# Kernel optimization log

Measured on AMD Instinct MI355X. Metric: run time of the kernel, lower is better.

The kernel has to match this reference:

```python
import jax, jax.numpy as jnp
import numpy as np


def _greedy_nms_single(scores, suppress):
    """Greedy score-ordered suppression for one scene.
    scores: [P] float max class score; suppress: [P, P] bool, row i suppresses col j
    (same class AND within class radius of point i). Returns keep mask [P] bool."""
    P = scores.shape[0]

    def cond(state):
        alive, _ = state
        return jnp.any(alive)

    def body(state):
        alive, keep = state
        i = jnp.argmax(jnp.where(alive, scores, -jnp.inf))  # highest-score remaining
        keep = keep.at[i].set(True)
        alive = alive & ~suppress[i]   # drop same-class points within radius of i
        alive = alive.at[i].set(False)
        return alive, keep

    alive0 = jnp.ones((P,), dtype=bool)
    keep0 = jnp.zeros((P,), dtype=bool)
    _, keep = jax.lax.while_loop(cond, body, (alive0, keep0))
    return keep


def _keep_mask(centers, cls_preds, class_radius):
    # centers: [B,P,3], cls_preds: [B,P,K], class_radius: [K]
    scores = jnp.max(cls_preds, axis=-1)     # [B,P]  torch.max(..., dim=1) values
    labels = jnp.argmax(cls_preds, axis=-1)  # [B,P]  torch.max(..., dim=1) indices
    diff = centers[:, :, None, :] - centers[:, None, :, :]        # [B,P,P,3]
    dist = jnp.sqrt(jnp.sum(diff * diff, axis=-1))                # [B,P,P] torch.norm
    same_class = labels[:, :, None] == labels[:, None, :]         # [B,P,P]
    radii = class_radius[labels]                                  # [B,P] radius of keeper i
    suppress = same_class & (dist < radii[:, :, None])            # [B,P,P]
    return jax.vmap(_greedy_nms_single)(scores, suppress)         # [B,P] bool


def setup_inputs() -> dict:
    key = jax.random.key(0)
    k1, k2, k3, k4 = jax.random.split(key, 4)
    B, P, C, K = 8, 2048, 1024, 3
    centers = jax.random.normal(k1, (B, P, 3), dtype=jnp.float32)
    features = jax.random.normal(k2, (B, P, C), dtype=jnp.float32)
    cls_preds = jax.random.normal(k3, (B, P, K), dtype=jnp.float32)
    class_radius = jax.random.uniform(k4, (K,), dtype=jnp.float32)  # per-class NMS radius
    return {"centers": centers, "features": features, "cls_preds": cls_preds,
            "class_radius": class_radius}


def reference(centers, features, cls_preds, class_radius):
    """Greedy per-class radius-based keypoint suppression (fixed-shape variant):
    instead of dynamically gathering kept points (data-dependent shape), we return
    the boolean keep mask and the inputs with suppressed entries zeroed out."""
    keep = _keep_mask(centers, cls_preds, class_radius)      # [B,P] bool
    m = keep[..., None].astype(features.dtype)
    return (centers * m, features * m, cls_preds * m, keep)
```

## Files before the change

### kernel.cpp

```cpp
#include <hip/hip_runtime.h>

#define B 8
#define P 2048
#define C 1024
#define NCHUNK 32
#define FEAT4 (B*P*C/4)
#define CEN4  (B*P*3/4)

typedef unsigned long long u64;
typedef unsigned int u32;

__global__ __launch_bounds__(512) void rank_kernel(
    const float* __restrict__ centers,
    const float* __restrict__ cls_preds,
    float4* __restrict__ scent,
    int* __restrict__ sidx)
{
    __shared__ u64 s_keys[P];
    __shared__ u32 s_cnt[64][9];
    const int b = blockIdx.x >> 5, gi = blockIdx.x & 31;
    const int tid = threadIdx.x, wv = tid >> 6, lane = tid & 63;
    const float* clsb = cls_preds + (size_t)b * P * 3;
    const float* cenb = centers + (size_t)b * P * 3;

    for (int e = tid; e < P; e += 512) {
        float s0 = clsb[e*3], s1 = clsb[e*3+1], s2 = clsb[e*3+2];
        float sc = s0; int lb = 0;
        if (s1 > sc) { sc = s1; lb = 1; }
        if (s2 > sc) { sc = s2; lb = 2; }
        u32 ub = __float_as_uint(sc);
        u32 ord = (ub & 0x80000000u) ? ~ub : (ub | 0x80000000u);
        s_keys[e] = ((u64)(~ord) << 32) | (u32)((e << 2) | lb);
    }
    __syncthreads();

    const u64 myk = s_keys[(gi << 6) + lane];
    u32 c = 0;
    const int sbase = wv << 8;
    #pragma unroll 8
    for (int u = 0; u < 256; ++u)
        c += (s_keys[sbase + u] < myk) ? 1u : 0u;
    s_cnt[lane][wv] = c;
    __syncthreads();

    if (wv == 0) {
        u32 rank = 0;
        #pragma unroll
        for (int s = 0; s < 8; ++s) rank += s_cnt[lane][s];
        u32 lo = (u32)myk;
        int orig = (int)(lo >> 2);
        float4 cc;
        cc.x = cenb[orig*3]; cc.y = cenb[orig*3+1]; cc.z = cenb[orig*3+2];
        cc.w = __int_as_float((int)(lo & 3));
        scent[(size_t)b * P + rank] = cc;
        sidx[(size_t)b * P + rank] = (int)lo;
    }
}

__global__ __launch_bounds__(512) void matrix_kernel(
    const float4* __restrict__ scent,
    const float* __restrict__ class_radius,
    u32* __restrict__ matT)
{
    __shared__ float4 s_cent[P];
    const int b = blockIdx.x >> 5, gi = blockIdx.x & 31;
    const int tid = threadIdx.x, wv = tid >> 6, lane = tid & 63;

    const float4 cj = scent[(size_t)b * P + (gi << 6) + lane];
    const int labj = __float_as_int(cj.w);
    const float r = class_radius[labj];
    const float r2 = r * r;
    const int wmin = gi << 1;

    for (int i = tid; i < P; i += 512) s_cent[i] = scent[(size_t)b * P + i];
    __syncthreads();

    for (int w = wv; w < 64; w += 8) {
        if (w < wmin) continue;
        u32 acc = 0;
        #pragma unroll
        for (int u = 0; u < 32; ++u) {
            float4 ci = s_cent[(w << 5) + u];
            float dx = cj.x - ci.x, dy = cj.y - ci.y, dz = cj.z - ci.z;
            bool sup = (__float_as_int(ci.w) == labj)
                       && (dx*dx + dy*dy + dz*dz < r2);
            acc |= ((u32)sup) << u;
        }
        matT[((size_t)b * 64 + w) * P + (gi << 6) + lane] = acc;
    }
}

__global__ __launch_bounds__(576) void scan_kernel(
    const u32* __restrict__ matT,
    const int* __restrict__ sidx,
    float* __restrict__ out_keep)
{
    __shared__ u32 s_tile[4][64][65];
    __shared__ u32 s_removed[64];
    __shared__ int s_sidx[P];
    const int b = blockIdx.x;
    const int tid = threadIdx.x, wv = tid >> 6, lane = tid & 63;
    const u32* mb = matT + (size_t)b * 64 * P;

    for (int i = tid; i < P; i += 576) s_sidx[i] = sidx[(size_t)b * P + i];
    if (tid < 64) s_removed[tid] = 0;
    if (wv >= 1) {
        #pragma unroll
        for (int c = 0; c < 3; ++c) {
            #pragma unroll
            for (int rr = 0; rr < 8; ++rr) {
                int w = ((wv - 1) << 3) + rr;
                s_tile[c][lane][w] = mb[(size_t)w * P + (c << 6) + lane];
            }
        }
    }
    __syncthreads();

    for (int g = 0; g < NCHUNK; ++g) {
        const int buf = g & 3;
        if (wv >= 1 && g + 3 < NCHUNK) {
            const int nb = (g + 3) << 6;
            #pragma unroll
            for (int rr = 0; rr < 8; ++rr) {
                int w = ((wv - 1) << 3) + rr;
                s_tile[(g + 3) & 3][lane][w] = mb[(size_t)w * P + nb + lane];
            }
        }
        if (wv == 0) {
            const int base = g << 6;
            u64 row = (u64)s_tile[buf][lane][2*g]
                    | ((u64)s_tile[buf][lane][2*g + 1] << 32);
            u64 rem = (u64)s_removed[2*g] | ((u64)s_removed[2*g + 1] << 32);
            u64 alive = ~rem;
            const u64 below = (1ull << lane) - 1ull;
            u64 keepm = 0;
            while (alive) {
                bool ok = ((alive >> lane) & 1ull) && ((row & alive & below) == 0ull);
                u64 newk = __ballot(ok);
                keepm |= newk;
                bool dead = (row & newk) != 0ull;
                u64 deadm = __ballot(dead);
                alive &= ~(newk | deadm);
            }
            int orig = s_sidx[base + lane] >> 2;
            out_keep[(size_t)b * P + orig] = ((keepm >> lane) & 1ull) ? 1.0f : 0.0f;
            u32 acc = 0;
            u64 m = keepm;
            while (m) {
                int q = (int)__ffsll((long long)m) - 1;
                acc |= s_tile[buf][q][lane];
                m &= m - 1ull;
            }
            s_removed[lane] |= acc;
        }
        __syncthreads();
    }
}

__global__ __launch_bounds__(256) void mask_kernel(
    const float* __restrict__ centers,
    const float* __restrict__ features,
    const float* __restrict__ cls_preds,
    const float* __restrict__ keep,
    float* __restrict__ out_centers,
    float* __restrict__ out_feat,
    float* __restrict__ out_cls)
{
    const int idx = blockIdx.x * 256 + threadIdx.x;
    if (idx < FEAT4) {
        const int row = idx >> 8;
        const float m = keep[row];
        float4 v = ((const float4*)features)[idx];
        v.x *= m; v.y *= m; v.z *= m; v.w *= m;
        ((float4*)out_feat)[idx] = v;
    } else if (idx < FEAT4 + CEN4) {
        const int q = idx - FEAT4;
        float4 v = ((const float4*)centers)[q];
        const int e = q * 4;
        v.x *= keep[(e    ) / 3]; v.y *= keep[(e + 1) / 3];
        v.z *= keep[(e + 2) / 3]; v.w *= keep[(e + 3) / 3];
        ((float4*)out_centers)[q] = v;
    } else if (idx < FEAT4 + 2 * CEN4) {
        const int q = idx - FEAT4 - CEN4;
        float4 v = ((const float4*)cls_preds)[q];
        const int e = q * 4;
        v.x *= keep[(e    ) / 3]; v.y *= keep[(e + 1) / 3];
        v.z *= keep[(e + 2) / 3]; v.w *= keep[(e + 3) / 3];
        ((float4*)out_cls)[q] = v;
    }
}

extern "C" void kernel_launch(void* const* d_in, const int* in_sizes, int n_in,
                              void* d_out, int out_size, void* d_ws, size_t ws_size,
                              hipStream_t stream) {
    const float* centers      = (const float*)d_in[0];
    const float* features     = (const float*)d_in[1];
    const float* cls_preds    = (const float*)d_in[2];
    const float* class_radius = (const float*)d_in[3];

    float* out = (float*)d_out;
    float* out_centers = out;
    float* out_feat    = out + (size_t)B * P * 3;
    float* out_cls     = out_feat + (size_t)B * P * C;
    float* out_keep    = out_cls + (size_t)B * P * 3;

    u32*    matT  = (u32*)out_feat;
    float4* scent = (float4*)(out_feat + 1048576);
    int*    sidx  = (int*)(out_feat + 1048576 + 65536);

    hipLaunchKernelGGL(rank_kernel, dim3(B * 32), dim3(512), 0, stream,
                       centers, cls_preds, scent, sidx);
    hipLaunchKernelGGL(matrix_kernel, dim3(B * 32), dim3(512), 0, stream,
                       scent, class_radius, matT);
    hipLaunchKernelGGL(scan_kernel, dim3(B), dim3(576), 0, stream,
                       matT, sidx, out_keep);
    hipLaunchKernelGGL(mask_kernel, dim3((FEAT4 + 2 * CEN4 + 255) / 256), dim3(256),
                       0, stream,
                       centers, features, cls_preds, out_keep,
                       out_centers, out_feat, out_cls);
}
```

Before: 181.1 us.

## Parallelize suppression-row OR across waves with register-held matrix tiles

The scan kernel drops the shared-memory transpose tile. Each helper wave now prefetches its slice of the suppression matrix into registers with vector loads, while wave 0 loads only its diagonal words. After wave 0 resolves a chunk's keep mask, the other eight waves OR the rows of the kept points in parallel into the removed mask using shared atomics. This replaces wave 0's serial ffs loop over shared-memory rows. The keep output is written in one pass at the end. In exchange it adds a second block barrier per chunk and uses strided, poorly coalesced global loads for the prefetch.

Result: faster. 173.0 us (-4.4%).

```diff
diff --git a/kernel.cpp b/kernel.cpp
--- a/kernel.cpp
+++ b/kernel.cpp
@@ -95,41 +95,49 @@
     const int* __restrict__ sidx,
     float* __restrict__ out_keep)
 {
-    __shared__ u32 s_tile[4][64][65];
+    __shared__ int s_sidx[P];
     __shared__ u32 s_removed[64];
-    __shared__ int s_sidx[P];
+    __shared__ u64 s_keepm[NCHUNK];
     const int b = blockIdx.x;
     const int tid = threadIdx.x, wv = tid >> 6, lane = tid & 63;
     const u32* mb = matT + (size_t)b * 64 * P;
 
     for (int i = tid; i < P; i += 576) s_sidx[i] = sidx[(size_t)b * P + i];
     if (tid < 64) s_removed[tid] = 0;
-    if (wv >= 1) {
-        #pragma unroll
-        for (int c = 0; c < 3; ++c) {
-            #pragma unroll
-            for (int rr = 0; rr < 8; ++rr) {
-                int w = ((wv - 1) << 3) + rr;
-                s_tile[c][lane][w] = mb[(size_t)w * P + (c << 6) + lane];
+
+    uint4 Va[4], Vb[4];
+    u32 Ra[4], Rb[4];
+    const int qb = (wv - 1) << 3;
+
+    #pragma unroll
+    for (int c = 0; c < 3; ++c) {
+        if (wv >= 1) {
+            const u32* p = mb + (size_t)lane * P + (c << 6) + qb;
+            Va[c] = *(const uint4*)p;
+            Vb[c] = *(const uint4*)(p + 4);
+        } else {
+            Ra[c] = mb[(size_t)(2*c    ) * P + (c << 6) + lane];
+            Rb[c] = mb[(size_t)(2*c + 1) * P + (c << 6) + lane];
+        }
+    }
+    __syncthreads();
+
+    #pragma unroll
+    for (int g = 0; g < NCHUNK; ++g) {
+        const int slot = g & 3;
+        if (g + 3 < NCHUNK) {
+            const int c = g + 3, ns = c & 3;
+            if (wv >= 1) {
+                const u32* p = mb + (size_t)lane * P + (c << 6) + qb;
+                Va[ns] = *(const uint4*)p;
+                Vb[ns] = *(const uint4*)(p + 4);
+            } else {
+                Ra[ns] = mb[(size_t)(2*c    ) * P + (c << 6) + lane];
+                Rb[ns] = mb[(size_t)(2*c + 1) * P + (c << 6) + lane];
             }
         }
-    }
-    __syncthreads();
-
-    for (int g = 0; g < NCHUNK; ++g) {
-        const int buf = g & 3;
-        if (wv >= 1 && g + 3 < NCHUNK) {
-            const int nb = (g + 3) << 6;
-            #pragma unroll
-            for (int rr = 0; rr < 8; ++rr) {
-                int w = ((wv - 1) << 3) + rr;
-                s_tile[(g + 3) & 3][lane][w] = mb[(size_t)w * P + nb + lane];
-            }
-        }
         if (wv == 0) {
-            const int base = g << 6;
-            u64 row = (u64)s_tile[buf][lane][2*g]
-                    | ((u64)s_tile[buf][lane][2*g + 1] << 32);
+            u64 row = (u64)Ra[slot] | ((u64)Rb[slot] << 32);
             u64 rem = (u64)s_removed[2*g] | ((u64)s_removed[2*g + 1] << 32);
             u64 alive = ~rem;
             const u64 below = (1ull << lane) - 1ull;
@@ -142,18 +150,29 @@
                 u64 deadm = __ballot(dead);
                 alive &= ~(newk | deadm);
             }
-            int orig = s_sidx[base + lane] >> 2;
-            out_keep[(size_t)b * P + orig] = ((keepm >> lane) & 1ull) ? 1.0f : 0.0f;
+            if (lane == 0) s_keepm[g] = keepm;
+        }
+        __syncthreads();
+        if (wv >= 1) {
+            const u32 kb = (u32)(s_keepm[g] >> qb) & 0xffu;
             u32 acc = 0;
-            u64 m = keepm;
-            while (m) {
-                int q = (int)__ffsll((long long)m) - 1;
-                acc |= s_tile[buf][q][lane];
-                m &= m - 1ull;
-            }
-            s_removed[lane] |= acc;
+            if (kb & 0x01u) acc |= Va[slot].x;
+            if (kb & 0x02u) acc |= Va[slot].y;
+            if (kb & 0x04u) acc |= Va[slot].z;
+            if (kb & 0x08u) acc |= Va[slot].w;
+            if (kb & 0x10u) acc |= Vb[slot].x;
+            if (kb & 0x20u) acc |= Vb[slot].y;
+            if (kb & 0x40u) acc |= Vb[slot].z;
+            if (kb & 0x80u) acc |= Vb[slot].w;
+            if (acc) atomicOr(&s_removed[lane], acc);
         }
         __syncthreads();
+    }
+
+    for (int pos = tid; pos < P; pos += 576) {
+        u64 km = s_keepm[pos >> 6];
+        int orig = s_sidx[pos] >> 2;
+        out_keep[(size_t)b * P + orig] = ((km >> (pos & 63)) & 1ull) ? 1.0f : 0.0f;
     }
 }
 
```
